# Performance work log

Measured on AMD Instinct MI355X. Metric: run time of the kernel, lower is better.

The kernel has to match this reference:

```python
import jax, jax.numpy as jnp
import numpy as np

NUM_HEADS = 4
NUM_POINTS = 8


def deform_attn_3d(q, value, ref, Hf, Wf, Wv, bv, Wo, bo, Wa, ba):
    # q: (BS,N,C)  value: (BS,Hf*Wf,C)  ref: (BS,N,D,2) normalized (x,y) in [0,1]
    BS, N, C = q.shape
    H, P = NUM_HEADS, NUM_POINTS
    D = ref.shape[2]
    c = C // H
    # value projection, split heads: (BS,H,M,c)
    v = (value @ Wv + bv).reshape(BS, Hf * Wf, H, c).transpose(0, 2, 1, 3)
    # sampling offsets and attention weights from the query
    off = (q @ Wo + bo).reshape(BS, N, H, P, 2)
    attn = jax.nn.softmax((q @ Wa + ba).reshape(BS, N, H, P), axis=-1)
    # normalize offsets by (W,H); distribute P points over D z-anchors (P//D per anchor)
    norm = jnp.array([Wf, Hf], dtype=q.dtype)
    off = off.reshape(BS, N, H, P // D, D, 2) / norm
    loc = (ref[:, :, None, None, :, :] + off).reshape(BS, N, H, P, 2)
    # grid_sample(align_corners=False, padding=zeros): pixel = loc*size - 0.5
    x = loc[..., 0] * Wf - 0.5
    y = loc[..., 1] * Hf - 0.5
    x0f = jnp.floor(x)
    y0f = jnp.floor(y)
    lx = x - x0f
    ly = y - y0f
    x0 = x0f.astype(jnp.int32)
    y0 = y0f.astype(jnp.int32)

    def tohead(a):  # (BS,N,H,P) -> (BS,H,N*P)
        return a.transpose(0, 2, 1, 3).reshape(BS, H, N * P)

    def gather(yy, xx):
        valid = ((xx >= 0) & (xx < Wf) & (yy >= 0) & (yy < Hf)).astype(q.dtype)
        idx = jnp.clip(yy, 0, Hf - 1) * Wf + jnp.clip(xx, 0, Wf - 1)
        g = jnp.take_along_axis(v, tohead(idx)[..., None], axis=2)  # (BS,H,N*P,c)
        return g * tohead(valid)[..., None]

    out = (gather(y0, x0) * tohead((1 - lx) * (1 - ly))[..., None]
           + gather(y0, x0 + 1) * tohead(lx * (1 - ly))[..., None]
           + gather(y0 + 1, x0) * tohead((1 - lx) * ly)[..., None]
           + gather(y0 + 1, x0 + 1) * tohead(lx * ly)[..., None])
    out = (out * tohead(attn)[..., None]).reshape(BS, H, N, P, c).sum(3)  # (BS,H,N,c)
    return out.transpose(0, 2, 1, 3).reshape(BS, N, C)


def spatial_cross_attention(query, query_pos, value, reference_points_cam, bev_mask,
                            Hf, Wf, Wv, bv, Wo, bo, Wa, ba, Wout, bout):
    # query/query_pos: (B,N,C); value: (S,M,B,C); ref: (S,B,N,D,2); bev_mask: (S,B,N,D)
    B, N, C = query.shape
    S, M = value.shape[0], value.shape[1]
    D = reference_points_cam.shape[3]
    q = query + query_pos
    # broadcast queries over cameras (mask-equivalent of the torch rebatch/compaction):
    # deformable attention is per-query independent, so computing all queries per cam
    # and masking invalid ones is the same math as rebatch+scatter.
    q_all = jnp.broadcast_to(q[:, None], (B, S, N, C)).reshape(B * S, N, C)
    v_all = value.transpose(2, 0, 1, 3).reshape(B * S, M, C)
    ref = reference_points_cam.transpose(1, 0, 2, 3, 4).reshape(B * S, N, D, 2)
    out = deform_attn_3d(q_all, v_all, ref, Hf, Wf, Wv, bv, Wo, bo, Wa, ba)
    out = out.reshape(B, S, N, C)
    mask_q = (bev_mask.sum(-1) > 0).astype(query.dtype)  # (S,B,N): query hits this cam
    slots = (out * mask_q.transpose(1, 0, 2)[..., None]).sum(1)  # (B,N,C)
    count = jnp.maximum(mask_q.sum(0), 1.0)  # (B,N) clamp(min=1)
    slots = slots / count[..., None]
    # output_proj, dropout (eval -> identity), residual with original query
    return slots @ Wout + bout + query


def setup_inputs() -> dict:
    B, S, N, Z, C = 1, 6, 16384, 8, 128
    Hf, Wf = 28, 50
    H, P = NUM_HEADS, NUM_POINTS
    rng = jax.random.key(0)
    ks = jax.random.split(rng, 12)
    return {
        "query": jax.random.normal(ks[0], (B, N, C), jnp.float32),
        "query_pos": 0.1 * jax.random.normal(ks[1], (B, N, C), jnp.float32),
        "value": jax.random.normal(ks[2], (S, Hf * Wf, B, C), jnp.float32),
        "reference_points_cam": jax.random.uniform(ks[3], (S, B, N, Z, 2), jnp.float32),
        "bev_mask": jax.random.randint(ks[4], (S, B, N, Z), 0, 2).astype(bool),
        "Wv": 0.02 * jax.random.normal(ks[5], (C, C), jnp.float32),
        "bv": jnp.zeros((C,), jnp.float32),
        "Wo": 0.02 * jax.random.normal(ks[6], (C, H * P * 2), jnp.float32),
        "bo": 0.5 * jax.random.normal(ks[7], (H * P * 2,), jnp.float32),
        "Wa": 0.02 * jax.random.normal(ks[8], (C, H * P), jnp.float32),
        "ba": jnp.zeros((H * P,), jnp.float32),
        "Wout": 0.02 * jax.random.normal(ks[9], (C, C), jnp.float32),
        "bout": jnp.zeros((C,), jnp.float32),
        "Hf": Hf,
        "Wf": Wf,
    }


def reference(query, query_pos, value, reference_points_cam, bev_mask,
              Wv, bv, Wo, bo, Wa, ba, Wout, bout, Hf, Wf):
    return spatial_cross_attention(query, query_pos, value, reference_points_cam, bev_mask,
                                   Hf, Wf, Wv, bv, Wo, bo, Wa, ba, Wout, bout)
```

## Files before the change

### kernel.cpp

```cpp
#include <hip/hip_runtime.h>

#define N_Q   16384
#define C_DIM 128
#define S_CAM 6
#define M_VAL 1400
#define D_Z   8
#define HF    28
#define WF    50
#define QPB   16

typedef float f32x2 __attribute__((ext_vector_type(2)));

__device__ __forceinline__ bool mask_any(const unsigned char* __restrict__ mask,
                                         int mflag, size_t mbase){
  if(mflag==0){
    int any=0;
    #pragma unroll
    for(int d=0;d<D_Z;d++) any |= mask[mbase+d];
    return any!=0;
  } else if(mflag==1){
    const int* mp = (const int*)mask;  int any=0;
    #pragma unroll
    for(int d=0;d<D_Z;d++) any |= mp[mbase+d];
    return any!=0;
  } else {
    const long long* mp = (const long long*)mask;  long long any=0;
    #pragma unroll
    for(int d=0;d<D_Z;d++) any |= mp[mbase+d];
    return any!=0;
  }
}

__device__ __forceinline__ void corner_acc(const uint4 cv, const float wgt,
                                           float* __restrict__ acc){
  const unsigned dw[4] = {cv.x, cv.y, cv.z, cv.w};
  #pragma unroll
  for(int j=0;j<4;j++){
    const f32x2 lo = __builtin_amdgcn_cvt_pk_f32_fp8(dw[j], false);
    const f32x2 hi = __builtin_amdgcn_cvt_pk_f32_fp8(dw[j], true);
    acc[j*4+0] += wgt*lo[0];  acc[j*4+1] += wgt*lo[1];
    acc[j*4+2] += wgt*hi[0];  acc[j*4+3] += wgt*hi[1];
  }
}

__global__ __launch_bounds__(256)
void value_proj_kernel(const float* __restrict__ value,
                       const float* __restrict__ Wv,
                       const float* __restrict__ bv,
                       unsigned char* __restrict__ v8,
                       const unsigned char* __restrict__ mask,
                       int* __restrict__ flag){
  __shared__ float tile[8][C_DIM];
  __shared__ int s_cntA, s_cntB;
  const int tid = threadIdx.x;
  const int col = tid & 127;
  const int rh  = tid >> 7;
  const int r0  = blockIdx.x * 8;
  if(blockIdx.x==0 && tid==0){ s_cntA=0; s_cntB=0; }
  {
    const float4* src = (const float4*)(value + (size_t)r0*C_DIM);
    ((float4*)&tile[0][0])[tid] = src[tid];
  }
  __syncthreads();
  float acc[4];
  const float bias = bv[col];
  #pragma unroll
  for(int r=0;r<4;r++) acc[r]=bias;
  for(int k=0;k<C_DIM;k+=4){
    const float w0 = Wv[(k+0)*C_DIM + col];
    const float w1 = Wv[(k+1)*C_DIM + col];
    const float w2 = Wv[(k+2)*C_DIM + col];
    const float w3 = Wv[(k+3)*C_DIM + col];
    #pragma unroll
    for(int r=0;r<4;r++){
      const float4 t = *(const float4*)&tile[rh*4+r][k];
      acc[r] += t.x*w0 + t.y*w1 + t.z*w2 + t.w*w3;
    }
  }
  #pragma unroll
  for(int r=0;r<4;r++){
    const int pk = __builtin_amdgcn_cvt_pk_fp8_f32(acc[r], acc[r], 0, false);
    v8[(size_t)(r0+rh*4+r)*C_DIM + col] = (unsigned char)(pk & 0xff);
  }
  if(blockIdx.x==0){
    int a=0, b=0;
    for(int i=tid;i<1024;i+=256){
      const unsigned char v = mask[i];
      if(((i&3)!=0) && v) a=1;
      if(((i&7)==4) && v) b=1;
    }
    if(a) atomicOr(&s_cntA,1);
    if(b) atomicOr(&s_cntB,1);
    __syncthreads();
    if(tid==0) flag[0] = s_cntA ? 0 : (s_cntB ? 1 : 2);
  }
}

__global__ __launch_bounds__(256)
void fused_deform_kernel(const unsigned char* __restrict__ v8,
                         const float* __restrict__ query,
                         const float* __restrict__ query_pos,
                         const float* __restrict__ Wo, const float* __restrict__ bo,
                         const float* __restrict__ Wa, const float* __restrict__ ba,
                         const float* __restrict__ ref,
                         const unsigned char* __restrict__ mask,
                         const int* __restrict__ flag,
                         const float* __restrict__ Wout,
                         const float* __restrict__ bout,
                         float* __restrict__ out){
  __shared__ float  qs[QPB][C_DIM+4];
  __shared__ float  offs[QPB][68];
  __shared__ float  attns[QPB][36];
  __shared__ float  logits[QPB][36];
  __shared__ float2 refs[QPB][S_CAM*D_Z+1];
  __shared__ int    activ[QPB][S_CAM];
  __shared__ float  cinv[QPB];

  const int tid = threadIdx.x;
  const int n0  = blockIdx.x * QPB;
  const int mflag = flag[0];
  const int qi = tid >> 4;
  const int l  = tid & 15;

  float2 rpre[3];
  #pragma unroll
  for(int j=0;j<3;j++){
    const int e = tid + 256*j;
    const int q = e/48, r = e%48;
    rpre[j] = ((const float2*)ref)[((size_t)(r>>3)*N_Q + (n0+q))*D_Z + (r&7)];
  }

  {
    const float4* qa = (const float4*)(query     + (size_t)n0*C_DIM);
    const float4* qb = (const float4*)(query_pos + (size_t)n0*C_DIM);
    #pragma unroll
    for(int j=0;j<2;j++){
      const int idx = tid + 256*j;
      const int r = idx >> 5, c4 = idx & 31;
      float4 A = qa[idx], B = qb[idx];
      *(float4*)&qs[r][c4*4] = make_float4(A.x+B.x, A.y+B.y, A.z+B.z, A.w+B.w);
    }
  }
  __syncthreads();

  {
    float ao0 = bo[l*4+0], ao1 = bo[l*4+1], ao2 = bo[l*4+2], ao3 = bo[l*4+3];
    float aa0 = ba[l*2+0], aa1 = ba[l*2+1];
    for(int k=0;k<C_DIM;k++){
      const float qv = qs[qi][k];
      const float4 wo = *(const float4*)&Wo[k*64 + l*4];
      const float2 wa = *(const float2*)&Wa[k*32 + l*2];
      ao0 += qv*wo.x; ao1 += qv*wo.y; ao2 += qv*wo.z; ao3 += qv*wo.w;
      aa0 += qv*wa.x; aa1 += qv*wa.y;
    }
    offs[qi][l*4+0] = ao0;  offs[qi][l*4+1] = ao1;
    offs[qi][l*4+2] = ao2;  offs[qi][l*4+3] = ao3;
    logits[qi][l*2+0] = aa0;  logits[qi][l*2+1] = aa1;
  }
  #pragma unroll
  for(int j=0;j<3;j++){
    const int e = tid + 256*j;
    refs[e/48][e%48] = rpre[j];
  }
  if(tid < QPB*S_CAM){
    const int q2 = tid / S_CAM, s = tid % S_CAM;
    activ[q2][s] = mask_any(mask, mflag, ((size_t)s*N_Q + (n0+q2))*D_Z) ? 1 : 0;
  }
  __syncthreads();
  if(tid < 64){
    const int q2 = tid >> 2, h = tid & 3;
    const float* L = &logits[q2][h*8];
    float mx = L[0];
    #pragma unroll
    for(int p=1;p<8;p++) mx = fmaxf(mx, L[p]);
    float e[8], ssum = 0.f;
    #pragma unroll
    for(int p=0;p<8;p++){ e[p] = __expf(L[p]-mx); ssum += e[p]; }
    const float inv = 1.f/ssum;
    #pragma unroll
    for(int p=0;p<8;p++) attns[q2][h*8+p] = e[p]*inv;
  } else if(tid >= 256-QPB){
    const int q2 = tid - (256-QPB);
    int c = 0;
    #pragma unroll
    for(int s=0;s<S_CAM;s++) c += activ[q2][s];
    cinv[q2] = 1.f / fmaxf((float)c, 1.f);
  }
  __syncthreads();

  const int sg  = l >> 3;
  const int ll  = l & 7;
  const int gch = ll*16;
  const int gh  = ll >> 1;
  float acc[16];
  #pragma unroll
  for(int i=0;i<16;i++) acc[i]=0.f;

  for(int s=sg*3; s<sg*3+3; s++){
    if(!activ[qi][s]) continue;
    const unsigned char* vb = v8 + (size_t)s*M_VAL*C_DIM + gch;
    #pragma unroll 2
    for(int p=0;p<8;p++){
      const float2 r2 = refs[qi][s*8+p];
      const float ox = offs[qi][gh*16+p*2+0];
      const float oy = offs[qi][gh*16+p*2+1];
      const float x = fmaf(r2.x, (float)WF, ox - 0.5f);
      const float y = fmaf(r2.y, (float)HF, oy - 0.5f);
      const float x0f = floorf(x), y0f = floorf(y);
      const float fx = x - x0f,    fy = y - y0f;
      const int x0 = (int)x0f, y0 = (int)y0f;
      const int x1 = x0+1,     y1 = y0+1;
      const float at = attns[qi][gh*8+p];
      const float wx0 = (x0>=0 && x0<WF) ? (1.f-fx) : 0.f;
      const float wx1 = (x1>=0 && x1<WF) ? fx       : 0.f;
      const float wy0 = ((y0>=0 && y0<HF) ? (1.f-fy) : 0.f) * at;
      const float wy1 = ((y1>=0 && y1<HF) ? fy       : 0.f) * at;
      const int x0c = min(max(x0,0), WF-1), x1c = min(max(x1,0), WF-1);
      const int y0c = min(max(y0,0), HF-1), y1c = min(max(y1,0), HF-1);
      const float w00 = wx0*wy0, w01 = wx1*wy0, w10 = wx0*wy1, w11 = wx1*wy1;
      const uint4 c00 = *(const uint4*)(vb + (size_t)(y0c*WF+x0c)*C_DIM);
      const uint4 c01 = *(const uint4*)(vb + (size_t)(y0c*WF+x1c)*C_DIM);
      const uint4 c10 = *(const uint4*)(vb + (size_t)(y1c*WF+x0c)*C_DIM);
      const uint4 c11 = *(const uint4*)(vb + (size_t)(y1c*WF+x1c)*C_DIM);
      corner_acc(c00, w00, acc);
      corner_acc(c01, w01, acc);
      corner_acc(c10, w10, acc);
      corner_acc(c11, w11, acc);
    }
  }

  __syncthreads();
  if(sg==0){
    #pragma unroll
    for(int i=0;i<4;i++)
      *(float4*)&qs[qi][gch+i*4] = *(const float4*)&acc[i*4];
  }
  __syncthreads();
  if(sg==1){
    const float inv = cinv[qi];
    #pragma unroll
    for(int i=0;i<4;i++){
      float4 pA = *(const float4*)&qs[qi][gch+i*4];
      *(float4*)&qs[qi][gch+i*4] = make_float4((pA.x+acc[i*4+0])*inv,
                                               (pA.y+acc[i*4+1])*inv,
                                               (pA.z+acc[i*4+2])*inv,
                                               (pA.w+acc[i*4+3])*inv);
    }
  }
  __syncthreads();
  {
    const int c0 = l*8;
    const int n  = n0 + qi;
    const float4 bA = *(const float4*)&bout[c0];
    const float4 bB = *(const float4*)&bout[c0+4];
    const float4 rA = *(const float4*)&query[(size_t)n*C_DIM + c0];
    const float4 rB = *(const float4*)&query[(size_t)n*C_DIM + c0 + 4];
    float o0=bA.x+rA.x, o1=bA.y+rA.y, o2=bA.z+rA.z, o3=bA.w+rA.w;
    float o4=bB.x+rB.x, o5=bB.y+rB.y, o6=bB.z+rB.z, o7=bB.w+rB.w;
    for(int k=0;k<C_DIM;k++){
      const float sv = qs[qi][k];
      const float4 wA = *(const float4*)&Wout[(size_t)k*C_DIM + c0];
      const float4 wB = *(const float4*)&Wout[(size_t)k*C_DIM + c0 + 4];
      o0 += sv*wA.x; o1 += sv*wA.y; o2 += sv*wA.z; o3 += sv*wA.w;
      o4 += sv*wB.x; o5 += sv*wB.y; o6 += sv*wB.z; o7 += sv*wB.w;
    }
    *(float4*)&out[(size_t)n*C_DIM + c0]     = make_float4(o0,o1,o2,o3);
    *(float4*)&out[(size_t)n*C_DIM + c0 + 4] = make_float4(o4,o5,o6,o7);
  }
}

extern "C" void kernel_launch(void* const* d_in, const int* in_sizes, int n_in,
                              void* d_out, int out_size, void* d_ws, size_t ws_size,
                              hipStream_t stream){
  const float* query     = (const float*)d_in[0];
  const float* query_pos = (const float*)d_in[1];
  const float* value     = (const float*)d_in[2];
  const float* ref       = (const float*)d_in[3];
  const unsigned char* mask = (const unsigned char*)d_in[4];
  const float* Wv   = (const float*)d_in[5];
  const float* bv   = (const float*)d_in[6];
  const float* Wo   = (const float*)d_in[7];
  const float* bo   = (const float*)d_in[8];
  const float* Wa   = (const float*)d_in[9];
  const float* ba   = (const float*)d_in[10];
  const float* Wout = (const float*)d_in[11];
  const float* bout = (const float*)d_in[12];
  float* out = (float*)d_out;

  int* flag = (int*)d_ws;
  unsigned char* v8 = (unsigned char*)((char*)d_ws + 64);

  value_proj_kernel<<<(S_CAM*M_VAL)/8, 256, 0, stream>>>(value, Wv, bv, v8, mask, flag);
  fused_deform_kernel<<<N_Q/QPB, 256, 0, stream>>>(v8, query, query_pos,
                                                   Wo, bo, Wa, ba, ref, mask, flag,
                                                   Wout, bout, out);
}
```

Before: 187.1 us.

## Halve queries per block, split sampling points across lanes, reduce with shuffles

Each block now handles 8 queries instead of 16, with 32 lanes per query. The lanes split both the camera groups and the sampling points, which doubles the grid and the parallelism in the gather phase. The cross-group partial sums are combined with wavefront xor shuffles instead of an LDS round-trip guarded by two block barriers. Bilinear accumulation uses packed two-wide float multiply-adds. The trade-off is more blocks that each re-read the projection weights, and a shuffle reduction over 16 accumulators per lane.

Result: no change. 189.8 us (+1.4%).

```diff
diff --git a/kernel.cpp b/kernel.cpp
--- a/kernel.cpp
+++ b/kernel.cpp
@@ -7,7 +7,7 @@
 #define D_Z   8
 #define HF    28
 #define WF    50
-#define QPB   16
+#define QPB   8
 
 typedef float f32x2 __attribute__((ext_vector_type(2)));
 
@@ -32,14 +32,13 @@
 }
 
 __device__ __forceinline__ void corner_acc(const uint4 cv, const float wgt,
-                                           float* __restrict__ acc){
+                                           f32x2* __restrict__ acc2){
+  const f32x2 w2 = {wgt, wgt};
   const unsigned dw[4] = {cv.x, cv.y, cv.z, cv.w};
   #pragma unroll
   for(int j=0;j<4;j++){
-    const f32x2 lo = __builtin_amdgcn_cvt_pk_f32_fp8(dw[j], false);
-    const f32x2 hi = __builtin_amdgcn_cvt_pk_f32_fp8(dw[j], true);
-    acc[j*4+0] += wgt*lo[0];  acc[j*4+1] += wgt*lo[1];
-    acc[j*4+2] += wgt*hi[0];  acc[j*4+3] += wgt*hi[1];
+    acc2[j*2+0] += w2 * __builtin_amdgcn_cvt_pk_f32_fp8(dw[j], false);
+    acc2[j*2+1] += w2 * __builtin_amdgcn_cvt_pk_f32_fp8(dw[j], true);
   }
 }
 
@@ -119,55 +118,54 @@
   const int tid = threadIdx.x;
   const int n0  = blockIdx.x * QPB;
   const int mflag = flag[0];
-  const int qi = tid >> 4;
-  const int l  = tid & 15;
-
-  float2 rpre[3];
-  #pragma unroll
-  for(int j=0;j<3;j++){
-    const int e = tid + 256*j;
-    const int q = e/48, r = e%48;
-    rpre[j] = ((const float2*)ref)[((size_t)(r>>3)*N_Q + (n0+q))*D_Z + (r&7)];
+  const int qi = tid >> 5;
+  const int l  = tid & 31;
+
+  float2 rpre0, rpre1;
+  {
+    const int q0 = tid/48, r0 = tid%48;
+    rpre0 = ((const float2*)ref)[((size_t)(r0>>3)*N_Q + (n0+q0))*D_Z + (r0&7)];
+    if(tid < 128){
+      const int e1 = tid + 256;
+      const int q1 = e1/48, r1 = e1%48;
+      rpre1 = ((const float2*)ref)[((size_t)(r1>>3)*N_Q + (n0+q1))*D_Z + (r1&7)];
+    }
   }
 
   {
     const float4* qa = (const float4*)(query     + (size_t)n0*C_DIM);
     const float4* qb = (const float4*)(query_pos + (size_t)n0*C_DIM);
-    #pragma unroll
-    for(int j=0;j<2;j++){
-      const int idx = tid + 256*j;
-      const int r = idx >> 5, c4 = idx & 31;
-      float4 A = qa[idx], B = qb[idx];
-      *(float4*)&qs[r][c4*4] = make_float4(A.x+B.x, A.y+B.y, A.z+B.z, A.w+B.w);
-    }
-  }
-  __syncthreads();
-
-  {
-    float ao0 = bo[l*4+0], ao1 = bo[l*4+1], ao2 = bo[l*4+2], ao3 = bo[l*4+3];
-    float aa0 = ba[l*2+0], aa1 = ba[l*2+1];
+    const int r = tid >> 5, c4 = tid & 31;
+    const float4 A = qa[tid], B = qb[tid];
+    *(float4*)&qs[r][c4*4] = make_float4(A.x+B.x, A.y+B.y, A.z+B.z, A.w+B.w);
+  }
+  __syncthreads();
+
+  {
+    float ao0 = bo[l*2+0], ao1 = bo[l*2+1];
+    float aa  = ba[l];
     for(int k=0;k<C_DIM;k++){
       const float qv = qs[qi][k];
-      const float4 wo = *(const float4*)&Wo[k*64 + l*4];
-      const float2 wa = *(const float2*)&Wa[k*32 + l*2];
-      ao0 += qv*wo.x; ao1 += qv*wo.y; ao2 += qv*wo.z; ao3 += qv*wo.w;
-      aa0 += qv*wa.x; aa1 += qv*wa.y;
-    }
-    offs[qi][l*4+0] = ao0;  offs[qi][l*4+1] = ao1;
-    offs[qi][l*4+2] = ao2;  offs[qi][l*4+3] = ao3;
-    logits[qi][l*2+0] = aa0;  logits[qi][l*2+1] = aa1;
-  }
-  #pragma unroll
-  for(int j=0;j<3;j++){
-    const int e = tid + 256*j;
-    refs[e/48][e%48] = rpre[j];
+      const float2 wo = *(const float2*)&Wo[k*64 + l*2];
+      const float  wa = Wa[k*32 + l];
+      ao0 += qv*wo.x; ao1 += qv*wo.y; aa += qv*wa;
+    }
+    offs[qi][l*2+0] = ao0;  offs[qi][l*2+1] = ao1;
+    logits[qi][l] = aa;
+  }
+  {
+    refs[tid/48][tid%48] = rpre0;
+    if(tid < 128){
+      const int e1 = tid + 256;
+      refs[e1/48][e1%48] = rpre1;
+    }
   }
   if(tid < QPB*S_CAM){
     const int q2 = tid / S_CAM, s = tid % S_CAM;
     activ[q2][s] = mask_any(mask, mflag, ((size_t)s*N_Q + (n0+q2))*D_Z) ? 1 : 0;
   }
   __syncthreads();
-  if(tid < 64){
+  if(tid < QPB*4){
     const int q2 = tid >> 2, h = tid & 3;
     const float* L = &logits[q2][h*8];
     float mx = L[0];
@@ -188,19 +186,21 @@
   }
   __syncthreads();
 
-  const int sg  = l >> 3;
+  const int pg  = l >> 4;
+  const int sg  = (l >> 3) & 1;
   const int ll  = l & 7;
   const int gch = ll*16;
   const int gh  = ll >> 1;
-  float acc[16];
-  #pragma unroll
-  for(int i=0;i<16;i++) acc[i]=0.f;
+  f32x2 acc2[8];
+  #pragma unroll
+  for(int i=0;i<8;i++) acc2[i] = (f32x2){0.f, 0.f};
 
   for(int s=sg*3; s<sg*3+3; s++){
     if(!activ[qi][s]) continue;
     const unsigned char* vb = v8 + (size_t)s*M_VAL*C_DIM + gch;
     #pragma unroll 2
-    for(int p=0;p<8;p++){
+    for(int pp=0;pp<4;pp++){
+      const int p = pg*4 + pp;
       const float2 r2 = refs[qi][s*8+p];
       const float ox = offs[qi][gh*16+p*2+0];
       const float oy = offs[qi][gh*16+p*2+1];
@@ -222,50 +222,38 @@
       const uint4 c01 = *(const uint4*)(vb + (size_t)(y0c*WF+x1c)*C_DIM);
       const uint4 c10 = *(const uint4*)(vb + (size_t)(y1c*WF+x0c)*C_DIM);
       const uint4 c11 = *(const uint4*)(vb + (size_t)(y1c*WF+x1c)*C_DIM);
-      corner_acc(c00, w00, acc);
-      corner_acc(c01, w01, acc);
-      corner_acc(c10, w10, acc);
-      corner_acc(c11, w11, acc);
-    }
-  }
-
-  __syncthreads();
-  if(sg==0){
+      corner_acc(c00, w00, acc2);
+      corner_acc(c01, w01, acc2);
+      corner_acc(c10, w10, acc2);
+      corner_acc(c11, w11, acc2);
+    }
+  }
+
+  float* accf = (float*)acc2;
+  #pragma unroll
+  for(int i=0;i<16;i++) accf[i] += __shfl_xor(accf[i], 16);
+  #pragma unroll
+  for(int i=0;i<16;i++) accf[i] += __shfl_xor(accf[i], 8);
+  if(l < 8){
+    const float inv = cinv[qi];
     #pragma unroll
     for(int i=0;i<4;i++)
-      *(float4*)&qs[qi][gch+i*4] = *(const float4*)&acc[i*4];
-  }
-  __syncthreads();
-  if(sg==1){
-    const float inv = cinv[qi];
-    #pragma unroll
-    for(int i=0;i<4;i++){
-      float4 pA = *(const float4*)&qs[qi][gch+i*4];
-      *(float4*)&qs[qi][gch+i*4] = make_float4((pA.x+acc[i*4+0])*inv,
-                                               (pA.y+acc[i*4+1])*inv,
-                                               (pA.z+acc[i*4+2])*inv,
-                                               (pA.w+acc[i*4+3])*inv);
-    }
-  }
-  __syncthreads();
-  {
-    const int c0 = l*8;
+      *(float4*)&qs[qi][gch+i*4] = make_float4(accf[i*4+0]*inv, accf[i*4+1]*inv,
+                                               accf[i*4+2]*inv, accf[i*4+3]*inv);
+  }
+
+  {
+    const int c0 = l*4;
     const int n  = n0 + qi;
     const float4 bA = *(const float4*)&bout[c0];
-    const float4 bB = *(const float4*)&bout[c0+4];
     const float4 rA = *(const float4*)&query[(size_t)n*C_DIM + c0];
-    const float4 rB = *(const float4*)&query[(size_t)n*C_DIM + c0 + 4];
     float o0=bA.x+rA.x, o1=bA.y+rA.y, o2=bA.z+rA.z, o3=bA.w+rA.w;
-    float o4=bB.x+rB.x, o5=bB.y+rB.y, o6=bB.z+rB.z, o7=bB.w+rB.w;
     for(int k=0;k<C_DIM;k++){
       const float sv = qs[qi][k];
       const float4 wA = *(const float4*)&Wout[(size_t)k*C_DIM + c0];
-      const float4 wB = *(const float4*)&Wout[(size_t)k*C_DIM + c0 + 4];
       o0 += sv*wA.x; o1 += sv*wA.y; o2 += sv*wA.z; o3 += sv*wA.w;
-      o4 += sv*wB.x; o5 += sv*wB.y; o6 += sv*wB.z; o7 += sv*wB.w;
-    }
-    *(float4*)&out[(size_t)n*C_DIM + c0]     = make_float4(o0,o1,o2,o3);
-    *(float4*)&out[(size_t)n*C_DIM + c0 + 4] = make_float4(o4,o5,o6,o7);
+    }
+    *(float4*)&out[(size_t)n*C_DIM + c0] = make_float4(o0,o1,o2,o3);
   }
 }
 
```
